# Optimization experiments

Hardware: AMD Instinct MI355X
Metric: run time of the kernel (lower is better)

## Reference

```python
import jax, jax.numpy as jnp
import numpy as np

H = 256  # hidden_channels
N_USERS = 100000
N_MOVIES = 50000
N_EDGES = 500000


def setup_inputs() -> dict:
    key = jax.random.key(0)
    k1, k2, k3, k4, k5, k6, k7 = jax.random.split(key, 7)
    user_emb = jax.random.normal(k1, (N_USERS, H), dtype=jnp.float32)
    movie_emb = jax.random.normal(k2, (N_MOVIES, H), dtype=jnp.float32)
    edge_label_index = jax.random.randint(k3, (2, N_EDGES), 0, N_MOVIES, dtype=jnp.int64)
    # Linear(2H, H) and Linear(H, 1) params, torch default init scale
    s1 = 1.0 / np.sqrt(2 * H)
    s2 = 1.0 / np.sqrt(H)
    W1 = jax.random.uniform(k4, (2 * H, H), dtype=jnp.float32, minval=-s1, maxval=s1)
    b1 = jax.random.uniform(k5, (H,), dtype=jnp.float32, minval=-s1, maxval=s1)
    W2 = jax.random.uniform(k6, (H, 1), dtype=jnp.float32, minval=-s2, maxval=s2)
    b2 = jax.random.uniform(k7, (1,), dtype=jnp.float32, minval=-s2, maxval=s2)
    return {"user_emb": user_emb, "movie_emb": movie_emb,
            "edge_label_index": edge_label_index,
            "W1": W1, "b1": b1, "W2": W2, "b2": b2}


def reference(user_emb, movie_emb, edge_label_index, W1, b1, W2, b2):
    u = user_emb[edge_label_index[0]]    # [E, H]
    m = movie_emb[edge_label_index[1]]   # [E, H]
    x = jnp.concatenate([u, m], axis=-1)  # [E, 2H]
    x = jax.nn.relu(x @ W1 + b1)          # [E, H]
    return x @ W2 + b2                    # [E, 1]
```

## Files before the change

kernel.cpp:

```cpp
#include <hip/hip_runtime.h>
#include <hip/hip_bf16.h>

typedef __attribute__((ext_vector_type(8))) short v8s;
typedef __attribute__((ext_vector_type(4))) float v4f;

constexpr int H  = 256;
constexpr int K2 = 512;
constexpr int XS = 72;
constexpr int WS = 72;

__device__ inline unsigned short f2bf(float f) {
    unsigned int u = __builtin_bit_cast(unsigned int, f);
    u += 0x7FFFu + ((u >> 16) & 1u);
    return (unsigned short)(u >> 16);
}
__device__ inline float bf2f(unsigned short s) {
    return __builtin_bit_cast(float, (unsigned int)s << 16);
}

__global__ void w1_transpose_kernel(const float* __restrict__ w1,
                                    unsigned short* __restrict__ w1t) {
    __shared__ float tile[32][33];
    const int bk = blockIdx.x;
    const int bn = blockIdx.y;
    const int tx = threadIdx.x & 31;
    const int ty8 = threadIdx.x >> 5;
#pragma unroll
    for (int i = 0; i < 4; ++i) {
        int ty = i * 8 + ty8;
        tile[ty][tx] = w1[(size_t)(bk * 32 + ty) * H + bn * 32 + tx];
    }
    __syncthreads();
#pragma unroll
    for (int i = 0; i < 4; ++i) {
        int ty = i * 8 + ty8;
        w1t[(size_t)(bn * 32 + ty) * K2 + bk * 32 + tx] = f2bf(tile[tx][ty]);
    }
}

__global__ __launch_bounds__(512) void emb_gemm_kernel(
    const float* __restrict__ emb,
    const unsigned short* __restrict__ w1t,
    const float* __restrict__ bias,
    unsigned short* __restrict__ outp,
    const int M, const int kofs)
{
    __shared__ unsigned short Xs[128 * XS];
    __shared__ unsigned short Wts[H * WS];

    const int t    = threadIdx.x;
    const int wave = t >> 6;
    const int lane = t & 63;
    const int wm   = wave >> 2;
    const int wn   = wave & 3;
    const int quad = lane >> 4;
    const int l16  = lane & 15;

    const long m0 = (long)blockIdx.x * 128;

    const int xr = t >> 2;
    const int xc = t & 3;
    long mr = m0 + xr; if (mr >= M) mr = M - 1;
    const float* arow = emb + (size_t)mr * H;

    const int wr  = t >> 3;
    const int wc8 = t & 7;

    v4f acc[4][4];
#pragma unroll
    for (int mt = 0; mt < 4; ++mt)
#pragma unroll
        for (int nt = 0; nt < 4; ++nt)
            acc[mt][nt] = (v4f){0.f, 0.f, 0.f, 0.f};

    for (int kt = 0; kt < 4; ++kt) {
        __syncthreads();
        {
            const float* s0 = arow + kt * 64 + xc * 8;
            v4f a0 = *(const v4f*)(s0);
            v4f a1 = *(const v4f*)(s0 + 4);
            v4f a2 = *(const v4f*)(s0 + 32);
            v4f a3 = *(const v4f*)(s0 + 36);
            v8s x0, x1;
#pragma unroll
            for (int i = 0; i < 4; ++i) { x0[i] = (short)f2bf(a0[i]); x0[4+i] = (short)f2bf(a1[i]); }
#pragma unroll
            for (int i = 0; i < 4; ++i) { x1[i] = (short)f2bf(a2[i]); x1[4+i] = (short)f2bf(a3[i]); }
            *(v8s*)(Xs + xr * XS + xc * 8)      = x0;
            *(v8s*)(Xs + xr * XS + xc * 8 + 32) = x1;
        }
#pragma unroll
        for (int j = 0; j < 4; ++j) {
            v8s wv = *(const v8s*)(w1t + (size_t)(j * 64 + wr) * K2 + kofs + kt * 64 + wc8 * 8);
            *(v8s*)(Wts + (j * 64 + wr) * WS + wc8 * 8) = wv;
        }
        __syncthreads();
#pragma unroll
        for (int ks = 0; ks < 2; ++ks) {
            v8s af[4], bf[4];
#pragma unroll
            for (int mt = 0; mt < 4; ++mt)
                af[mt] = *(const v8s*)(Xs + (wm * 64 + mt * 16 + l16) * XS + ks * 32 + quad * 8);
#pragma unroll
            for (int nt = 0; nt < 4; ++nt)
                bf[nt] = *(const v8s*)(Wts + (wn * 64 + nt * 16 + l16) * WS + ks * 32 + quad * 8);
#pragma unroll
            for (int mt = 0; mt < 4; ++mt)
#pragma unroll
                for (int nt = 0; nt < 4; ++nt)
                    acc[mt][nt] = __builtin_amdgcn_mfma_f32_16x16x32_bf16(
                        af[mt], bf[nt], acc[mt][nt], 0, 0, 0);
        }
    }

    float bv[4];
#pragma unroll
    for (int nt = 0; nt < 4; ++nt)
        bv[nt] = bias ? bias[wn * 64 + nt * 16 + l16] : 0.f;

#pragma unroll
    for (int mt = 0; mt < 4; ++mt) {
#pragma unroll
        for (int j = 0; j < 4; ++j) {
            long m = m0 + wm * 64 + mt * 16 + quad * 4 + j;
            if (m < M) {
#pragma unroll
                for (int nt = 0; nt < 4; ++nt) {
                    int n = wn * 64 + nt * 16 + l16;
                    outp[(size_t)m * H + n] = f2bf(acc[mt][nt][j] + bv[nt]);
                }
            }
        }
    }
}

__global__ __launch_bounds__(256, 8) void edge_score_kernel(
    const unsigned short* __restrict__ P,
    const unsigned short* __restrict__ Q,
    const int* __restrict__ eli,
    const float* __restrict__ w2,
    const float* __restrict__ b2,
    float* __restrict__ out,
    const int E, const int n_users, const int n_movies)
{
    const int t   = threadIdx.x;
    const int hw  = t >> 5;
    const int l32 = t & 31;

    float w2v[8];
    {
        v4f a = *(const v4f*)(w2 + l32 * 8);
        v4f b = *(const v4f*)(w2 + l32 * 8 + 4);
#pragma unroll
        for (int i = 0; i < 4; ++i) { w2v[i] = a[i]; w2v[4 + i] = b[i]; }
    }
    const float b2v = b2[0];
    const long base = (long)blockIdx.x * 64;

#pragma unroll
    for (int i = 0; i < 8; ++i) {
        long e = base + i * 8 + hw;
        const bool valid = (e < E);
        long ec = valid ? e : 0;
        int u = eli[ec];
        int m = eli[(long)E + ec];
        u = u < 0 ? 0 : (u >= n_users  ? n_users  - 1 : u);
        m = m < 0 ? 0 : (m >= n_movies ? n_movies - 1 : m);
        v8s pv = *(const v8s*)(P + (size_t)u * H + l32 * 8);
        v8s qv = *(const v8s*)(Q + (size_t)m * H + l32 * 8);
        float s = 0.f;
#pragma unroll
        for (int j = 0; j < 8; ++j) {
            float h = bf2f((unsigned short)pv[j]) + bf2f((unsigned short)qv[j]);
            h = h > 0.f ? h : 0.f;
            s += h * w2v[j];
        }
        s += __shfl_xor(s, 1, 64);
        s += __shfl_xor(s, 2, 64);
        s += __shfl_xor(s, 4, 64);
        s += __shfl_xor(s, 8, 64);
        s += __shfl_xor(s, 16, 64);
        if (l32 == 0 && valid) out[e] = s + b2v;
    }
}

constexpr int BMF = 64;
__global__ __launch_bounds__(512, 4) void edge_decoder_kernel(
    const float* __restrict__ user_emb, const float* __restrict__ movie_emb,
    const int* __restrict__ eli, const unsigned short* __restrict__ w1t,
    const float* __restrict__ b1, const float* __restrict__ w2,
    const float* __restrict__ b2, float* __restrict__ out,
    const int E, const int n_users, const int n_movies)
{
    __shared__ unsigned short Xs[BMF * XS];
    __shared__ unsigned short Wts[H * WS];
    __shared__ float red[4][BMF];
    const int t = threadIdx.x, wave = t >> 6, lane = t & 63;
    const int wm = wave >> 2, wn = wave & 3, quad = lane >> 4, l16 = lane & 15;
    const long e0 = (long)blockIdx.x * BMF;
    const int xr = t >> 3, xc = t & 7;
    long eg = e0 + xr; if (eg >= E) eg = 0;
    int iu = eli[eg], im = eli[(long)E + eg];
    iu = iu < 0 ? 0 : (iu >= n_users ? n_users - 1 : iu);
    im = im < 0 ? 0 : (im >= n_movies ? n_movies - 1 : im);
    const float* urow = user_emb + (size_t)iu * H;
    const float* mrow = movie_emb + (size_t)im * H;
    const int wr = t >> 3, wc8 = t & 7;
    const unsigned short* wbase = w1t + (size_t)wr * K2 + wc8 * 8;
    v4f acc[2][4];
#pragma unroll
    for (int mt = 0; mt < 2; ++mt)
#pragma unroll
        for (int nt = 0; nt < 4; ++nt) acc[mt][nt] = (v4f){0.f,0.f,0.f,0.f};
    v4f xq0 = *(const v4f*)(urow + xc * 8);
    v4f xq1 = *(const v4f*)(urow + xc * 8 + 4);
    v8s wq[4];
#pragma unroll
    for (int j = 0; j < 4; ++j) wq[j] = *(const v8s*)(wbase + (size_t)j * 64 * K2);
    for (int kt = 0; kt < 8; ++kt) {
        __syncthreads();
        { v8s xv;
#pragma unroll
          for (int i = 0; i < 4; ++i) xv[i] = (short)f2bf(xq0[i]);
#pragma unroll
          for (int i = 0; i < 4; ++i) xv[4+i] = (short)f2bf(xq1[i]);
          *(v8s*)(Xs + xr * XS + xc * 8) = xv; }
#pragma unroll
        for (int j = 0; j < 4; ++j) *(v8s*)(Wts + (j * 64 + wr) * WS + wc8 * 8) = wq[j];
        if (kt < 7) {
            const int kn = kt + 1, koff = (kn * 64) & 255;
            const float* src = ((kn < 4) ? urow : mrow) + koff + xc * 8;
            xq0 = *(const v4f*)(src); xq1 = *(const v4f*)(src + 4);
#pragma unroll
            for (int j = 0; j < 4; ++j) wq[j] = *(const v8s*)(wbase + (size_t)j * 64 * K2 + kn * 64);
        }
        __syncthreads();
#pragma unroll
        for (int ks = 0; ks < 2; ++ks) {
            v8s af[2], bf[4];
#pragma unroll
            for (int mt = 0; mt < 2; ++mt)
                af[mt] = *(const v8s*)(Xs + (wm * 32 + mt * 16 + l16) * XS + ks * 32 + quad * 8);
#pragma unroll
            for (int nt = 0; nt < 4; ++nt)
                bf[nt] = *(const v8s*)(Wts + (wn * 64 + nt * 16 + l16) * WS + ks * 32 + quad * 8);
#pragma unroll
            for (int mt = 0; mt < 2; ++mt)
#pragma unroll
                for (int nt = 0; nt < 4; ++nt)
                    acc[mt][nt] = __builtin_amdgcn_mfma_f32_16x16x32_bf16(af[mt], bf[nt], acc[mt][nt], 0, 0, 0);
        }
    }
    float b1v[4], w2v[4];
#pragma unroll
    for (int nt = 0; nt < 4; ++nt) {
        int n = wn * 64 + nt * 16 + l16;
        b1v[nt] = b1[n]; w2v[nt] = w2[n];
    }
    const float b2v = b2[0];
#pragma unroll
    for (int mt = 0; mt < 2; ++mt) {
        float s[4] = {0.f,0.f,0.f,0.f};
#pragma unroll
        for (int nt = 0; nt < 4; ++nt)
#pragma unroll
            for (int j = 0; j < 4; ++j) {
                float h = acc[mt][nt][j] + b1v[nt];
                h = h > 0.f ? h : 0.f;
                s[j] += h * w2v[nt];
            }
#pragma unroll
        for (int j = 0; j < 4; ++j) {
            float v = s[j];
            v += __shfl_xor(v, 1, 64); v += __shfl_xor(v, 2, 64);
            v += __shfl_xor(v, 4, 64); v += __shfl_xor(v, 8, 64);
            if (l16 == 0) red[wn][wm * 32 + mt * 16 + quad * 4 + j] = v;
        }
    }
    __syncthreads();
    if (t < BMF) {
        long e = e0 + t;
        if (e < E) out[e] = red[0][t] + red[1][t] + red[2][t] + red[3][t] + b2v;
    }
}

extern "C" void kernel_launch(void* const* d_in, const int* in_sizes, int n_in,
                              void* d_out, int out_size, void* d_ws, size_t ws_size,
                              hipStream_t stream) {
    const float* user_emb  = (const float*)d_in[0];
    const float* movie_emb = (const float*)d_in[1];
    const int*   eli       = (const int*)d_in[2];
    const float* w1        = (const float*)d_in[3];
    const float* b1        = (const float*)d_in[4];
    const float* w2        = (const float*)d_in[5];
    const float* b2        = (const float*)d_in[6];
    float*       out       = (float*)d_out;

    const int E        = out_size;
    const int n_users  = in_sizes[0] / H;
    const int n_movies = in_sizes[1] / H;

    unsigned short* w1t = (unsigned short*)d_ws;
    const size_t w1t_bytes = (size_t)K2 * H * 2;
    const size_t p_bytes   = (size_t)n_users  * H * 2;
    const size_t q_bytes   = (size_t)n_movies * H * 2;

    w1_transpose_kernel<<<dim3(16, 8), 256, 0, stream>>>(w1, w1t);

    if (ws_size >= w1t_bytes + p_bytes + q_bytes) {
        unsigned short* P = (unsigned short*)((char*)d_ws + w1t_bytes);
        unsigned short* Q = (unsigned short*)((char*)d_ws + w1t_bytes + p_bytes);
        emb_gemm_kernel<<<(n_users  + 127) / 128, 512, 0, stream>>>(
            user_emb,  w1t, b1,      P, n_users,  0);
        emb_gemm_kernel<<<(n_movies + 127) / 128, 512, 0, stream>>>(
            movie_emb, w1t, nullptr, Q, n_movies, 256);
        edge_score_kernel<<<(E + 63) / 64, 256, 0, stream>>>(
            P, Q, eli, w2, b2, out, E, n_users, n_movies);
    } else {
        edge_decoder_kernel<<<(E + BMF - 1) / BMF, 512, 0, stream>>>(
            user_emb, movie_emb, eli, w1t, b1, w2, b2, out, E, n_users, n_movies);
    }
}
```

Baseline: 298.4 us.

## Merge user/movie GEMMs into one launch, prefetch tiles, pipeline edge gathers

Merges the user and movie projection GEMMs into a single launch that picks its source by block index, and halves the row tile to 64 so more blocks fit per CU. Global loads for the next K tile of activations and weights are now issued before the MFMA loop, overlapping memory latency with compute. The edge-score kernel loads all indices up front and double-buffers the P/Q row gathers. Costs are more registers and less reuse of the weight tile per block.

New measurement: 286.5 us. -4.0%, faster.

```diff
diff --git a/kernel.cpp b/kernel.cpp
--- a/kernel.cpp
+++ b/kernel.cpp
@@ -38,15 +38,24 @@
     }
 }
 
-__global__ __launch_bounds__(512) void emb_gemm_kernel(
-    const float* __restrict__ emb,
+__global__ __launch_bounds__(512, 4) void emb_gemm_fused_kernel(
+    const float* __restrict__ user_emb,
+    const float* __restrict__ movie_emb,
     const unsigned short* __restrict__ w1t,
-    const float* __restrict__ bias,
-    unsigned short* __restrict__ outp,
-    const int M, const int kofs)
+    const float* __restrict__ b1,
+    unsigned short* __restrict__ P,
+    unsigned short* __restrict__ Q,
+    const int n_users, const int n_movies, const int nbu)
 {
-    __shared__ unsigned short Xs[128 * XS];
+    __shared__ unsigned short Xs[64 * XS];
     __shared__ unsigned short Wts[H * WS];
+
+    const int  isMovie = (blockIdx.x >= nbu) ? 1 : 0;
+    const float* emb  = isMovie ? movie_emb : user_emb;
+    unsigned short* outp = isMovie ? Q : P;
+    const int  M     = isMovie ? n_movies : n_users;
+    const int  kofs  = isMovie ? 256 : 0;
+    const long m0    = (long)(blockIdx.x - (isMovie ? nbu : 0)) * 64;
 
     const int t    = threadIdx.x;
     const int wave = t >> 6;
@@ -56,56 +65,60 @@
     const int quad = lane >> 4;
     const int l16  = lane & 15;
 
-    const long m0 = (long)blockIdx.x * 128;
-
-    const int xr = t >> 2;
-    const int xc = t & 3;
+    const int xr = t >> 3;
+    const int xc = t & 7;
     long mr = m0 + xr; if (mr >= M) mr = M - 1;
     const float* arow = emb + (size_t)mr * H;
 
     const int wr  = t >> 3;
     const int wc8 = t & 7;
-
-    v4f acc[4][4];
-#pragma unroll
-    for (int mt = 0; mt < 4; ++mt)
+    const unsigned short* wbase = w1t + (size_t)wr * K2 + kofs + wc8 * 8;
+
+    v4f acc[2][4];
+#pragma unroll
+    for (int mt = 0; mt < 2; ++mt)
 #pragma unroll
         for (int nt = 0; nt < 4; ++nt)
             acc[mt][nt] = (v4f){0.f, 0.f, 0.f, 0.f};
+
+    v4f a0 = *(const v4f*)(arow + xc * 8);
+    v4f a1 = *(const v4f*)(arow + xc * 8 + 4);
+    v8s wq[4];
+#pragma unroll
+    for (int j = 0; j < 4; ++j)
+        wq[j] = *(const v8s*)(wbase + (size_t)j * 64 * K2);
 
     for (int kt = 0; kt < 4; ++kt) {
         __syncthreads();
         {
-            const float* s0 = arow + kt * 64 + xc * 8;
-            v4f a0 = *(const v4f*)(s0);
-            v4f a1 = *(const v4f*)(s0 + 4);
-            v4f a2 = *(const v4f*)(s0 + 32);
-            v4f a3 = *(const v4f*)(s0 + 36);
-            v8s x0, x1;
-#pragma unroll
-            for (int i = 0; i < 4; ++i) { x0[i] = (short)f2bf(a0[i]); x0[4+i] = (short)f2bf(a1[i]); }
-#pragma unroll
-            for (int i = 0; i < 4; ++i) { x1[i] = (short)f2bf(a2[i]); x1[4+i] = (short)f2bf(a3[i]); }
-            *(v8s*)(Xs + xr * XS + xc * 8)      = x0;
-            *(v8s*)(Xs + xr * XS + xc * 8 + 32) = x1;
-        }
-#pragma unroll
-        for (int j = 0; j < 4; ++j) {
-            v8s wv = *(const v8s*)(w1t + (size_t)(j * 64 + wr) * K2 + kofs + kt * 64 + wc8 * 8);
-            *(v8s*)(Wts + (j * 64 + wr) * WS + wc8 * 8) = wv;
+            v8s xv;
+#pragma unroll
+            for (int i = 0; i < 4; ++i) { xv[i] = (short)f2bf(a0[i]); xv[4+i] = (short)f2bf(a1[i]); }
+            *(v8s*)(Xs + xr * XS + xc * 8) = xv;
+        }
+#pragma unroll
+        for (int j = 0; j < 4; ++j)
+            *(v8s*)(Wts + (j * 64 + wr) * WS + wc8 * 8) = wq[j];
+        if (kt < 3) {
+            const int kn = kt + 1;
+            a0 = *(const v4f*)(arow + kn * 64 + xc * 8);
+            a1 = *(const v4f*)(arow + kn * 64 + xc * 8 + 4);
+#pragma unroll
+            for (int j = 0; j < 4; ++j)
+                wq[j] = *(const v8s*)(wbase + (size_t)j * 64 * K2 + kn * 64);
         }
         __syncthreads();
 #pragma unroll
         for (int ks = 0; ks < 2; ++ks) {
-            v8s af[4], bf[4];
-#pragma unroll
-            for (int mt = 0; mt < 4; ++mt)
-                af[mt] = *(const v8s*)(Xs + (wm * 64 + mt * 16 + l16) * XS + ks * 32 + quad * 8);
+            v8s af[2], bf[4];
+#pragma unroll
+            for (int mt = 0; mt < 2; ++mt)
+                af[mt] = *(const v8s*)(Xs + (wm * 32 + mt * 16 + l16) * XS + ks * 32 + quad * 8);
 #pragma unroll
             for (int nt = 0; nt < 4; ++nt)
                 bf[nt] = *(const v8s*)(Wts + (wn * 64 + nt * 16 + l16) * WS + ks * 32 + quad * 8);
 #pragma unroll
-            for (int mt = 0; mt < 4; ++mt)
+            for (int mt = 0; mt < 2; ++mt)
 #pragma unroll
                 for (int nt = 0; nt < 4; ++nt)
                     acc[mt][nt] = __builtin_amdgcn_mfma_f32_16x16x32_bf16(
@@ -116,13 +129,13 @@
     float bv[4];
 #pragma unroll
     for (int nt = 0; nt < 4; ++nt)
-        bv[nt] = bias ? bias[wn * 64 + nt * 16 + l16] : 0.f;
-
-#pragma unroll
-    for (int mt = 0; mt < 4; ++mt) {
+        bv[nt] = isMovie ? 0.f : b1[wn * 64 + nt * 16 + l16];
+
+#pragma unroll
+    for (int mt = 0; mt < 2; ++mt) {
 #pragma unroll
         for (int j = 0; j < 4; ++j) {
-            long m = m0 + wm * 64 + mt * 16 + quad * 4 + j;
+            long m = m0 + wm * 32 + mt * 16 + quad * 4 + j;
             if (m < M) {
 #pragma unroll
                 for (int nt = 0; nt < 4; ++nt) {
@@ -157,17 +170,27 @@
     const float b2v = b2[0];
     const long base = (long)blockIdx.x * 64;
 
+    int us[8], ms[8];
 #pragma unroll
     for (int i = 0; i < 8; ++i) {
         long e = base + i * 8 + hw;
-        const bool valid = (e < E);
-        long ec = valid ? e : 0;
+        long ec = (e < E) ? e : 0;
         int u = eli[ec];
         int m = eli[(long)E + ec];
-        u = u < 0 ? 0 : (u >= n_users  ? n_users  - 1 : u);
-        m = m < 0 ? 0 : (m >= n_movies ? n_movies - 1 : m);
-        v8s pv = *(const v8s*)(P + (size_t)u * H + l32 * 8);
-        v8s qv = *(const v8s*)(Q + (size_t)m * H + l32 * 8);
+        us[i] = u < 0 ? 0 : (u >= n_users  ? n_users  - 1 : u);
+        ms[i] = m < 0 ? 0 : (m >= n_movies ? n_movies - 1 : m);
+    }
+
+    v8s pv = *(const v8s*)(P + (size_t)us[0] * H + l32 * 8);
+    v8s qv = *(const v8s*)(Q + (size_t)ms[0] * H + l32 * 8);
+
+#pragma unroll
+    for (int i = 0; i < 8; ++i) {
+        v8s pn, qn;
+        if (i < 7) {
+            pn = *(const v8s*)(P + (size_t)us[i + 1] * H + l32 * 8);
+            qn = *(const v8s*)(Q + (size_t)ms[i + 1] * H + l32 * 8);
+        }
         float s = 0.f;
 #pragma unroll
         for (int j = 0; j < 8; ++j) {
@@ -180,7 +203,9 @@
         s += __shfl_xor(s, 4, 64);
         s += __shfl_xor(s, 8, 64);
         s += __shfl_xor(s, 16, 64);
-        if (l32 == 0 && valid) out[e] = s + b2v;
+        long e = base + i * 8 + hw;
+        if (l32 == 0 && e < E) out[e] = s + b2v;
+        pv = pn; qv = qn;
     }
 }
 
@@ -310,10 +335,10 @@
     if (ws_size >= w1t_bytes + p_bytes + q_bytes) {
         unsigned short* P = (unsigned short*)((char*)d_ws + w1t_bytes);
         unsigned short* Q = (unsigned short*)((char*)d_ws + w1t_bytes + p_bytes);
-        emb_gemm_kernel<<<(n_users  + 127) / 128, 512, 0, stream>>>(
-            user_emb,  w1t, b1,      P, n_users,  0);
-        emb_gemm_kernel<<<(n_movies + 127) / 128, 512, 0, stream>>>(
-            movie_emb, w1t, nullptr, Q, n_movies, 256);
+        const int nbu = (n_users  + 63) / 64;
+        const int nbm = (n_movies + 63) / 64;
+        emb_gemm_fused_kernel<<<nbu + nbm, 512, 0, stream>>>(
+            user_emb, movie_emb, w1t, b1, P, Q, n_users, n_movies, nbu);
         edge_score_kernel<<<(E + 63) / 64, 256, 0, stream>>>(
             P, Q, eli, w2, b2, out, E, n_users, n_movies);
     } else {
```
